# Performance work log

Measured on AMD Instinct MI355X. Metric: run time of the kernel, lower is better.

Reference implementation:

```python
import jax, jax.numpy as jnp
import numpy as np
import math

B, S, DIN, DOUT, H, L, R, E = 8, 512, 256, 256, 8, 4, 8, 65536
N = B * S  # graph nodes = all tokens
DEPTH = DOUT // H


def setup_inputs() -> dict:
    key = jax.random.key(0)
    ks = jax.random.split(key, 16)
    s_in = 1.0 / math.sqrt(DIN)
    s_out = 1.0 / math.sqrt(DOUT)
    return {
        "x": jax.random.normal(ks[0], (B, S, DIN), jnp.float32),
        # graph structure (constant ints)
        "edge_src": jax.random.randint(ks[1], (E,), 0, N),
        "edge_dst": jax.random.randint(ks[2], (E,), 0, N),
        "edge_type": jax.random.randint(ks[3], (E,), 0, R),
        # linear: input_size -> output_size
        "Wl": jax.random.normal(ks[4], (DOUT, DIN), jnp.float32) * s_in,
        "bl": jnp.zeros((DOUT,), jnp.float32),
        # relational GAT params per layer / relation
        "Wgat": jax.random.normal(ks[5], (L, R, DOUT, DOUT), jnp.float32) * s_out,
        "a_src": jax.random.normal(ks[6], (L, R, DOUT), jnp.float32) * s_out,
        "a_dst": jax.random.normal(ks[7], (L, R, DOUT), jnp.float32) * s_out,
        # linear1: output_size -> input_size
        "W1": jax.random.normal(ks[8], (DIN, DOUT), jnp.float32) * s_out,
        "b1": jnp.zeros((DIN,), jnp.float32),
        # Wq, Wk: input_size -> output_size
        "Wq": jax.random.normal(ks[9], (DOUT, DIN), jnp.float32) * s_in,
        "bq": jnp.zeros((DOUT,), jnp.float32),
        "Wk": jax.random.normal(ks[10], (DOUT, DIN), jnp.float32) * s_in,
        "bk": jnp.zeros((DOUT,), jnp.float32),
    }


def _segment_softmax(e, dst, n):
    m = jax.ops.segment_max(e, dst, num_segments=n)
    ex = jnp.exp(e - m[dst])
    denom = jax.ops.segment_sum(ex, dst, num_segments=n)
    return ex / (denom[dst] + 1e-16)


def _rgat(h, Wgat, a_src, a_dst, edge_src, edge_dst, edge_type):
    # h: [N, DOUT]
    for l in range(L):
        # per-relation transform of all nodes: [R, N, D]
        hr = jnp.einsum('nd,rde->rne', h, Wgat[l])
        msg = hr[edge_type, edge_src]  # [E, D] gather by (relation, src)
        logits = (jnp.sum(a_src[l][edge_type] * msg, axis=-1)
                  + jnp.sum(a_dst[l][edge_type] * h[edge_dst], axis=-1))
        alpha = _segment_softmax(jax.nn.leaky_relu(logits, 0.2), edge_dst, N)
        agg = jax.ops.segment_sum(alpha[:, None] * msg, edge_dst, num_segments=N)
        h = jax.nn.elu(agg)
    return h


def reference(x, edge_src, edge_dst, edge_type, Wl, bl, Wgat, a_src, a_dst,
              W1, b1, Wq, bq, Wk, bk):
    h = x @ Wl.T + bl                       # [B, S, DOUT]
    h = h.reshape(N, DOUT)
    h = _rgat(h, Wgat, a_src, a_dst, edge_src, edge_dst, edge_type)
    h = h.reshape(B, S, DOUT)
    h = h @ W1.T + b1                       # [B, S, DIN]
    q = (h @ Wq.T + bq).reshape(B, S, H, DEPTH).transpose(0, 2, 1, 3)
    k = (h @ Wk.T + bk).reshape(B, S, H, DEPTH).transpose(0, 2, 1, 3)
    attn = jnp.einsum('bhqd,bhkd->bhqk', q, k) / math.sqrt(DEPTH)
    return attn
```

## Files before the change

kernel.cpp:

```cpp
#include <hip/hip_runtime.h>
#include <math.h>

#define NN 4096
#define D 256
#define RR 8
#define LL 4
#define EE 65536
#define BB 8
#define SS 512
#define HH 8
#define RK 256
#define RN 2048

typedef short bf16x8 __attribute__((ext_vector_type(8)));
typedef float f32x4 __attribute__((ext_vector_type(4)));

__device__ __forceinline__ unsigned short f2bf(float f) {
  unsigned u = __float_as_uint(f);
  unsigned r = (u + 0x7fffu + ((u >> 16) & 1u)) >> 16;
  return (unsigned short)r;
}
__device__ __forceinline__ float bf2f(unsigned short s) {
  return __uint_as_float(((unsigned)s) << 16);
}

__device__ __forceinline__ void gload16(unsigned short* dst, const unsigned short* src) {
  __builtin_amdgcn_global_load_lds(
      (const __attribute__((address_space(1))) void*)src,
      (__attribute__((address_space(3))) void*)dst, 16, 0, 0);
}

template<int BM, int BN, bool F32OUT, bool SPLITOUT>
__device__ __forceinline__ void gemm_body(unsigned short* lds, int bx, int by,
    const unsigned short* __restrict__ Ah, const unsigned short* __restrict__ Al,
    const unsigned short* __restrict__ Bh, const unsigned short* __restrict__ Bl,
    const float* __restrict__ bias,
    float* __restrict__ C, unsigned short* __restrict__ Ch, unsigned short* __restrict__ Cl,
    int M, int N, int K)
{
  constexpr int MF = BM / 32;
  constexpr int NF = BN / 32;
  constexpr int ABUF = BM * 32;
  constexpr int BBUF = BN * 32;
  constexpr int BUFSZ = 2 * ABUF + 2 * BBUF;

  const int t = threadIdx.x;
  const int lane = t & 63;
  const int w = t >> 6;
  const int wm = w >> 1, wn = w & 1;
  const int rb = by * BM;
  const int cb = bx * BN;

  f32x4 acc[MF][NF];
#pragma unroll
  for (int m = 0; m < MF; ++m)
#pragma unroll
    for (int n = 0; n < NF; ++n)
      acc[m][n] = (f32x4){0.f, 0.f, 0.f, 0.f};

  const int srow = t >> 2;
  const int lslot = (t & 3) ^ ((srow >> 1) & 3);
  const unsigned short* gAh = Ah + (size_t)(rb + srow) * K + lslot * 8;
  const unsigned short* gAl = Al + (size_t)(rb + srow) * K + lslot * 8;
  const unsigned short* gBh = Bh + (size_t)(cb + srow) * K + lslot * 8;
  const unsigned short* gBl = Bl + (size_t)(cb + srow) * K + lslot * 8;

  auto stage = [&](int buf, int k0) {
    unsigned short* p = lds + buf * BUFSZ;
#pragma unroll
    for (int i = 0; i < BM / 64; ++i) {
      gload16(p + i * 2048 + t * 8,        gAh + (size_t)i * 64 * K + k0);
      gload16(p + ABUF + i * 2048 + t * 8, gAl + (size_t)i * 64 * K + k0);
    }
#pragma unroll
    for (int i = 0; i < BN / 64; ++i) {
      gload16(p + 2 * ABUF + i * 2048 + t * 8,        gBh + (size_t)i * 64 * K + k0);
      gload16(p + 2 * ABUF + BBUF + i * 2048 + t * 8, gBl + (size_t)i * 64 * K + k0);
    }
  };

  stage(0, 0);
  int cur = 0;
  for (int k0 = 0; k0 < K; k0 += 32) {
    __syncthreads();
    if (k0 + 32 < K) stage(cur ^ 1, k0 + 32);
    const unsigned short* p = lds + cur * BUFSZ;

    bf16x8 ah[MF], al[MF];
#pragma unroll
    for (int m = 0; m < MF; ++m) {
      int row = wm * (BM / 2) + m * 16 + (lane & 15);
      int off = row * 32 + (((lane >> 4) ^ ((row >> 1) & 3)) << 3);
      ah[m] = *(const bf16x8*)(p + off);
      al[m] = *(const bf16x8*)(p + ABUF + off);
    }
#pragma unroll
    for (int n = 0; n < NF; ++n) {
      int brow = wn * (BN / 2) + n * 16 + (lane & 15);
      int boff = brow * 32 + (((lane >> 4) ^ ((brow >> 1) & 3)) << 3);
      bf16x8 bh = *(const bf16x8*)(p + 2 * ABUF + boff);
      bf16x8 bl = *(const bf16x8*)(p + 2 * ABUF + BBUF + boff);
#pragma unroll
      for (int m = 0; m < MF; ++m) {
        acc[m][n] = __builtin_amdgcn_mfma_f32_16x16x32_bf16(ah[m], bh, acc[m][n], 0, 0, 0);
        acc[m][n] = __builtin_amdgcn_mfma_f32_16x16x32_bf16(al[m], bh, acc[m][n], 0, 0, 0);
        acc[m][n] = __builtin_amdgcn_mfma_f32_16x16x32_bf16(ah[m], bl, acc[m][n], 0, 0, 0);
      }
    }
    cur ^= 1;
  }

#pragma unroll
  for (int m = 0; m < MF; ++m) {
#pragma unroll
    for (int n = 0; n < NF; ++n) {
      int row0 = rb + wm * (BM / 2) + m * 16 + (lane >> 4) * 4;
      int col = cb + wn * (BN / 2) + n * 16 + (lane & 15);
      float bv = bias ? bias[col] : 0.f;
#pragma unroll
      for (int j = 0; j < 4; ++j) {
        float v = acc[m][n][j] + bv;
        size_t idx = (size_t)(row0 + j) * N + col;
        if (F32OUT) C[idx] = v;
        if (SPLITOUT) {
          unsigned short hb = f2bf(v);
          Ch[idx] = hb;
          Cl[idx] = f2bf(v - bf2f(hb));
        }
      }
    }
  }
}

template<int BM, int BN, bool F32OUT, bool SPLITOUT>
__global__ __launch_bounds__(256) void gemm_split(
    const unsigned short* __restrict__ Ah, const unsigned short* __restrict__ Al,
    const unsigned short* __restrict__ Bh, const unsigned short* __restrict__ Bl,
    const float* __restrict__ bias,
    float* __restrict__ C, unsigned short* __restrict__ Ch, unsigned short* __restrict__ Cl,
    int M, int N, int K)
{
  __shared__ unsigned short lds[2 * (2 * BM * 32 + 2 * BN * 32)];
  gemm_body<BM, BN, F32OUT, SPLITOUT>(lds, blockIdx.x, blockIdx.y,
      Ah, Al, Bh, Bl, bias, C, Ch, Cl, M, N, K);
}

__global__ __launch_bounds__(256) void fill_gemm1_k(
    const int* __restrict__ ed, int* __restrict__ cur, int* __restrict__ csr,
    const unsigned short* __restrict__ xh, const unsigned short* __restrict__ xl,
    const unsigned short* __restrict__ wlh, const unsigned short* __restrict__ wll,
    const float* __restrict__ bl,
    unsigned short* __restrict__ hh, unsigned short* __restrict__ hl)
{
  __shared__ unsigned short lds[2 * (2 * 64 * 32 + 2 * 64 * 32)];
  int b = blockIdx.x;
  if (b < 256) {
    int e = b * 256 + threadIdx.x;
    int p = atomicAdd(&cur[ed[e]], 1);
    csr[p] = e;
  } else {
    int b2 = b - 256;
    gemm_body<64, 64, false, true>(lds, b2 & 3, b2 >> 2,
        xh, xl, wlh, wll, bl, nullptr, hh, hl, NN, D, D);
  }
}

__global__ __launch_bounds__(256) void rgat_scores_k(
    const unsigned short* __restrict__ Ah, const unsigned short* __restrict__ Al,
    const unsigned short* __restrict__ Bh, const unsigned short* __restrict__ Bl,
    float* __restrict__ C,
    const float* __restrict__ wa_l, const float* __restrict__ adst_l,
    float* __restrict__ ssrc, float* __restrict__ sdst)
{
  __shared__ unsigned short lds[2 * (2 * 128 * 32 + 2 * 128 * 32)];
  const int b = blockIdx.x;
  const int t = threadIdx.x;
  if (b < 512) {
    gemm_body<128, 128, true, false>(lds, b & 15, b >> 4,
        Ah, Al, Bh, Bl, nullptr, C, nullptr, nullptr, NN, RN, RK);
  } else {
    float* sh = (float*)lds;
    int n = b - 512;
    size_t idx = (size_t)n * D + t;
    sh[t] = bf2f(Ah[idx]) + bf2f(Al[idx]);
    __syncthreads();
    int lane = t & 63, wv = t >> 6;
#pragma unroll
    for (int rr = 0; rr < 2; ++rr) {
      int r = wv * 2 + rr;
      const float* wr = wa_l + (size_t)r * D;
      const float* ar = adst_l + (size_t)r * D;
      float s1 = sh[lane] * wr[lane] + sh[lane+64] * wr[lane+64]
               + sh[lane+128] * wr[lane+128] + sh[lane+192] * wr[lane+192];
      float s2 = sh[lane] * ar[lane] + sh[lane+64] * ar[lane+64]
               + sh[lane+128] * ar[lane+128] + sh[lane+192] * ar[lane+192];
#pragma unroll
      for (int o = 32; o; o >>= 1) { s1 += __shfl_down(s1, o); s2 += __shfl_down(s2, o); }
      if (lane == 0) { ssrc[(size_t)r * NN + n] = s1; sdst[(size_t)r * NN + n] = s2; }
    }
  }
}

__global__ __launch_bounds__(1024) void scan_k(const int* __restrict__ cnt,
    int* __restrict__ off, int* __restrict__ cur) {
  __shared__ int part[1024];
  int t = threadIdx.x;
  int base = t * 4;
  int c0 = cnt[base], c1 = cnt[base+1], c2 = cnt[base+2], c3 = cnt[base+3];
  int s = c0 + c1 + c2 + c3;
  part[t] = s;
  __syncthreads();
  for (int o = 1; o < 1024; o <<= 1) {
    int v = 0;
    if (t >= o) v = part[t - o];
    __syncthreads();
    part[t] += v;
    __syncthreads();
  }
  int excl = part[t] - s;
  off[base] = excl; off[base+1] = excl + c0; off[base+2] = excl + c0 + c1;
  off[base+3] = excl + c0 + c1 + c2;
  cur[base] = excl; cur[base+1] = excl + c0; cur[base+2] = excl + c0 + c1;
  cur[base+3] = excl + c0 + c1 + c2;
  if (t == 1023) off[NN] = EE;
}

__global__ __launch_bounds__(256) void prep_k(
    const float* __restrict__ x, unsigned short* __restrict__ xh, unsigned short* __restrict__ xl,
    const float* __restrict__ Wl, unsigned short* __restrict__ wlh, unsigned short* __restrict__ wll,
    const float* __restrict__ Wq, const float* __restrict__ Wk, const float* __restrict__ W1,
    unsigned short* __restrict__ fqkh, unsigned short* __restrict__ fqkl,
    const float* __restrict__ b1, const float* __restrict__ bq, const float* __restrict__ bk,
    float* __restrict__ bqk,
    const float* __restrict__ Wgat, const float* __restrict__ asrc,
    unsigned short* __restrict__ th, unsigned short* __restrict__ tl,
    float* __restrict__ wa,
    const int* __restrict__ ed, int* __restrict__ cnt)
{
  __shared__ float s[32][33];
  int b = blockIdx.x, t = threadIdx.x;
  if (b < 1088) {
    const float* src; unsigned short* hi; unsigned short* lo; int i;
    if (b < 1024) { src = x;  hi = xh;  lo = xl;  i = b * 256 + t; }
    else          { src = Wl; hi = wlh; lo = wll; i = (b - 1024) * 256 + t; }
    float4 v = ((const float4*)src)[i];
    ushort4 h, l;
    h.x = f2bf(v.x); l.x = f2bf(v.x - bf2f(h.x));
    h.y = f2bf(v.y); l.y = f2bf(v.y - bf2f(h.y));
    h.z = f2bf(v.z); l.z = f2bf(v.z - bf2f(h.z));
    h.w = f2bf(v.w); l.w = f2bf(v.w - bf2f(h.w));
    ((ushort4*)hi)[i] = h;
    ((ushort4*)lo)[i] = l;
  } else if (b < 1600) {
    int b2 = b - 1088;
    int j = (b2 & 3) * 64 + (t & 63);
    int i = (b2 >> 2) * 4 + (t >> 6);
    const float* row = i < 256 ? Wq + (size_t)i * D : Wk + (size_t)(i - 256) * D;
    float sm = 0.f;
    for (int k = 0; k < D; ++k) sm += row[k] * W1[(size_t)k * D + j];
    size_t idx = (size_t)i * D + j;
    unsigned short hb = f2bf(sm);
    fqkh[idx] = hb;
    fqkl[idx] = f2bf(sm - bf2f(hb));
  } else if (b < 1728) {
    int b2 = b - 1600;
    int idx = b2 * 4 + (t >> 6);
    int lane = t & 63;
    const float* row = idx < 256 ? Wq + (size_t)idx * D : Wk + (size_t)(idx - 256) * D;
    float sm = 0.f;
    for (int i = lane; i < D; i += 64) sm += row[i] * b1[i];
#pragma unroll
    for (int o = 32; o; o >>= 1) sm += __shfl_down(sm, o);
    if (lane == 0) bqk[idx] = sm + (idx < 256 ? bq[idx] : bk[idx - 256]);
  } else if (b < 3776) {
    int b2 = b - 1728;
    int g = b2 >> 6, bi = (b2 >> 3) & 7, bj = b2 & 7;
    int r = t >> 3, c = (t & 7) * 4;
    float4 v = *(const float4*)(Wgat + ((size_t)g * D + bi * 32 + r) * D + bj * 32 + c);
    s[r][c + 0] = v.x; s[r][c + 1] = v.y; s[r][c + 2] = v.z; s[r][c + 3] = v.w;
    __syncthreads();
    size_t ob = ((size_t)g * D + bj * 32 + r) * D + bi * 32 + c;
    ushort4 h, l4;
    float o0 = s[c + 0][r], o1 = s[c + 1][r], o2 = s[c + 2][r], o3 = s[c + 3][r];
    h.x = f2bf(o0); l4.x = f2bf(o0 - bf2f(h.x));
    h.y = f2bf(o1); l4.y = f2bf(o1 - bf2f(h.y));
    h.z = f2bf(o2); l4.z = f2bf(o2 - bf2f(h.z));
    h.w = f2bf(o3); l4.w = f2bf(o3 - bf2f(h.w));
    *(ushort4*)(th + ob) = h;
    *(ushort4*)(tl + ob) = l4;
    if (t < 32) {
      const float* av = asrc + (size_t)g * D + bj * 32;
      float p2 = 0.f;
#pragma unroll
      for (int cc = 0; cc < 32; ++cc) p2 += s[t][cc] * av[cc];
      atomicAdd(&wa[(size_t)g * D + bi * 32 + t], p2);
    }
  } else {
    int e = (b - 3776) * 256 + t;
    atomicAdd(&cnt[ed[e]], 1);
  }
}

__global__ __launch_bounds__(256) void agg_fused_k(
    const int* __restrict__ csr, const int* __restrict__ off,
    const int* __restrict__ et, const int* __restrict__ es,
    const float* __restrict__ ssrc, const float* __restrict__ sdst,
    const float* __restrict__ hr2,
    unsigned short* __restrict__ hh, unsigned short* __restrict__ hl,
    const float* __restrict__ wa_next, const float* __restrict__ adst_next,
    float* __restrict__ ssrc_o, float* __restrict__ sdst_o)
{
  __shared__ float slog[1024];
  __shared__ int soff[1024];
  __shared__ float sdn[RR];
  __shared__ float red[8];
  __shared__ float wred[4][256];
  int n = blockIdx.x, tid = threadIdx.x;
  int o0 = off[n];
  int deg = off[n + 1] - o0;
  if (deg > 1024) deg = 1024;
  if (tid < RR) sdn[tid] = sdst[(size_t)tid * NN + n];
  __syncthreads();
  for (int i = tid; i < deg; i += 256) {
    int e = csr[o0 + i];
    int t = et[e], s = es[e];
    float v = ssrc[(size_t)t * NN + s] + sdn[t];
    slog[i] = v > 0.f ? v : 0.2f * v;
    soff[i] = s * (RR * D) + t * D;
  }
  __syncthreads();
  int lane = tid & 63, wv = tid >> 6;
  float lm = -INFINITY;
  for (int i = tid; i < deg; i += 256) lm = fmaxf(lm, slog[i]);
#pragma unroll
  for (int o = 32; o; o >>= 1) lm = fmaxf(lm, __shfl_xor(lm, o));
  if (lane == 0) red[wv] = lm;
  __syncthreads();
  float m = fmaxf(fmaxf(red[0], red[1]), fmaxf(red[2], red[3]));
  float ls = 0.f;
  for (int i = tid; i < deg; i += 256) {
    float a = expf(slog[i] - m);
    slog[i] = a;
    ls += a;
  }
#pragma unroll
  for (int o = 32; o; o >>= 1) ls += __shfl_xor(ls, o);
  if (lane == 0) red[4 + wv] = ls;
  __syncthreads();
  float dinv = 1.f / (red[4] + red[5] + red[6] + red[7] + 1e-16f);
  float4 a4 = make_float4(0.f, 0.f, 0.f, 0.f);
  for (int i = wv; i < deg; i += 4) {
    float al = slog[i];
    float4 rv = ((const float4*)(hr2 + (size_t)soff[i]))[lane];
    a4.x += al * rv.x; a4.y += al * rv.y; a4.z += al * rv.z; a4.w += al * rv.w;
  }
  ((float4*)wred[wv])[lane] = a4;
  __syncthreads();
  float acc = (wred[0][tid] + wred[1][tid]) + (wred[2][tid] + wred[3][tid]);
  acc *= dinv;
  float v = acc > 0.f ? acc : expm1f(acc);
  size_t idx = (size_t)n * D + tid;
  unsigned short hb = f2bf(v);
  hh[idx] = hb;
  hl[idx] = f2bf(v - bf2f(hb));

  if (wa_next) {
    __syncthreads();
    slog[tid] = v;
    __syncthreads();
#pragma unroll
    for (int rr2 = 0; rr2 < 2; ++rr2) {
      int r = wv * 2 + rr2;
      const float* wr = wa_next + (size_t)r * D;
      const float* ar = adst_next + (size_t)r * D;
      float s1 = slog[lane] * wr[lane] + slog[lane+64] * wr[lane+64]
               + slog[lane+128] * wr[lane+128] + slog[lane+192] * wr[lane+192];
      float s2 = slog[lane] * ar[lane] + slog[lane+64] * ar[lane+64]
               + slog[lane+128] * ar[lane+128] + slog[lane+192] * ar[lane+192];
#pragma unroll
      for (int o = 32; o; o >>= 1) { s1 += __shfl_down(s1, o); s2 += __shfl_down(s2, o); }
      if (lane == 0) { ssrc_o[(size_t)r * NN + n] = s1; sdst_o[(size_t)r * NN + n] = s2; }
    }
  }
}

__global__ __launch_bounds__(256) void attn_mfma_k(
    const unsigned short* __restrict__ qkh, const unsigned short* __restrict__ qkl,
    float* __restrict__ out)
{
  int bh = blockIdx.y; int b = bh >> 3, hd = bh & 7;
  int rb = (blockIdx.x >> 3) * 64, cb = (blockIdx.x & 7) * 64;
  int t = threadIdx.x, lane = t & 63, w = t >> 6;
  int wm = w >> 1, wn = w & 1;
  int colq = hd * 32 + (lane >> 4) * 8;
  int colk = 256 + colq;
  int arow = b * SS + rb + wm * 32 + (lane & 15);
  int brow = b * SS + cb + wn * 32 + (lane & 15);

  bf16x8 aH[2], aL[2], bH[2], bL[2];
#pragma unroll
  for (int m = 0; m < 2; ++m) {
    size_t o1 = (size_t)(arow + m * 16) * 512 + colq;
    aH[m] = *(const bf16x8*)(qkh + o1);
    aL[m] = *(const bf16x8*)(qkl + o1);
    size_t o2 = (size_t)(brow + m * 16) * 512 + colk;
    bH[m] = *(const bf16x8*)(qkh + o2);
    bL[m] = *(const bf16x8*)(qkl + o2);
  }
  f32x4 acc[2][2];
#pragma unroll
  for (int m = 0; m < 2; ++m)
#pragma unroll
    for (int n = 0; n < 2; ++n) {
      acc[m][n] = (f32x4){0.f, 0.f, 0.f, 0.f};
      acc[m][n] = __builtin_amdgcn_mfma_f32_16x16x32_bf16(aH[m], bH[n], acc[m][n], 0, 0, 0);
      acc[m][n] = __builtin_amdgcn_mfma_f32_16x16x32_bf16(aL[m], bH[n], acc[m][n], 0, 0, 0);
      acc[m][n] = __builtin_amdgcn_mfma_f32_16x16x32_bf16(aH[m], bL[n], acc[m][n], 0, 0, 0);
    }
  const float scale = 0.17677669529663687f;
  size_t ob = (size_t)bh * SS * SS;
#pragma unroll
  for (int m = 0; m < 2; ++m)
#pragma unroll
    for (int n = 0; n < 2; ++n) {
      int row0 = rb + wm * 32 + m * 16 + (lane >> 4) * 4;
      int col = cb + wn * 32 + n * 16 + (lane & 15);
#pragma unroll
      for (int j = 0; j < 4; ++j)
        out[ob + (size_t)(row0 + j) * SS + col] = acc[m][n][j] * scale;
    }
}

extern "C" void kernel_launch(void* const* d_in, const int* in_sizes, int n_in,
                              void* d_out, int out_size, void* d_ws, size_t ws_size,
                              hipStream_t stream) {
  const float* x    = (const float*)d_in[0];
  const int*   es   = (const int*)d_in[1];
  const int*   ed   = (const int*)d_in[2];
  const int*   et   = (const int*)d_in[3];
  const float* Wl   = (const float*)d_in[4];
  const float* bl   = (const float*)d_in[5];
  const float* Wgat = (const float*)d_in[6];
  const float* asr  = (const float*)d_in[7];
  const float* adt  = (const float*)d_in[8];
  const float* W1   = (const float*)d_in[9];
  const float* b1   = (const float*)d_in[10];
  const float* Wq   = (const float*)d_in[11];
  const float* bq   = (const float*)d_in[12];
  const float* Wk   = (const float*)d_in[13];
  const float* bk   = (const float*)d_in[14];
  float* out = (float*)d_out;

  char* w = (char*)d_ws;
  size_t o = 0;
  auto alloc = [&](size_t bytes) { void* p = w + o; o += (bytes + 255) & ~(size_t)255; return p; };
  unsigned short* hh    = (unsigned short*)alloc((size_t)NN * D * 2);
  unsigned short* hl    = (unsigned short*)alloc((size_t)NN * D * 2);
  unsigned short* Wgt_h = (unsigned short*)alloc((size_t)LL * RR * D * D * 2);
  unsigned short* Wgt_l = (unsigned short*)alloc((size_t)LL * RR * D * D * 2);
  unsigned short* wlh   = (unsigned short*)alloc((size_t)D * D * 2);
  unsigned short* wll   = (unsigned short*)alloc((size_t)D * D * 2);
  unsigned short* fqkh  = (unsigned short*)alloc((size_t)2 * D * D * 2);
  unsigned short* fqkl  = (unsigned short*)alloc((size_t)2 * D * D * 2);
  float* bqk   = (float*)alloc((size_t)2 * D * 4);
  int*   cnt   = (int*)alloc((size_t)NN * 4);
  float* wa    = (float*)alloc((size_t)LL * RR * D * 4);
  float* ssrcA = (float*)alloc((size_t)RR * NN * 4);
  float* sdstA = (float*)alloc((size_t)RR * NN * 4);
  float* ssrcB = (float*)alloc((size_t)RR * NN * 4);
  float* sdstB = (float*)alloc((size_t)RR * NN * 4);
  int*   off   = (int*)alloc((size_t)(NN + 1) * 4);
  int*   cur   = (int*)alloc((size_t)NN * 4);
  int*   csr   = (int*)alloc((size_t)EE * 4);
  char* big = (char*)alloc((size_t)NN * RR * D * 4);
  float*          hr2 = (float*)big;
  unsigned short* xh  = (unsigned short*)big;
  unsigned short* xl  = (unsigned short*)(big + (size_t)NN * D * 2);
  unsigned short* qkh = (unsigned short*)big;
  unsigned short* qkl = (unsigned short*)(big + (size_t)NN * 512 * 2);

  hipMemsetAsync(cnt, 0, (size_t)NN * 4 + (size_t)LL * RR * D * 4, stream);

  prep_k<<<4032, 256, 0, stream>>>(x, xh, xl, Wl, wlh, wll, Wq, Wk, W1,
                                   fqkh, fqkl, b1, bq, bk, bqk,
                                   Wgat, asr, Wgt_h, Wgt_l, wa, ed, cnt);
  scan_k<<<1, 1024, 0, stream>>>(cnt, off, cur);
  fill_gemm1_k<<<512, 256, 0, stream>>>(ed, cur, csr, xh, xl, wlh, wll, bl, hh, hl);

  for (int l = 0; l < LL; ++l) {
    int grid = (l == 0) ? 512 + NN : 512;
    rgat_scores_k<<<grid, 256, 0, stream>>>(
        hh, hl, Wgt_h + (size_t)l * RR * D * D, Wgt_l + (size_t)l * RR * D * D,
        hr2, wa, adt, ssrcA, sdstA);
    const float* wan = (l < LL - 1) ? wa + (size_t)(l + 1) * RR * D : nullptr;
    const float* adn = (l < LL - 1) ? adt + (size_t)(l + 1) * RR * D : nullptr;
    const float* sin_ = (l & 1) ? ssrcB : ssrcA;
    const float* din_ = (l & 1) ? sdstB : sdstA;
    float* sou_ = (l & 1) ? ssrcA : ssrcB;
    float* dou_ = (l & 1) ? sdstA : sdstB;
    agg_fused_k<<<NN, 256, 0, stream>>>(csr, off, et, es, sin_, din_, hr2,
                                        hh, hl, wan, adn, sou_, dou_);
  }

  gemm_split<64, 64, false, true><<<dim3(8, 64), 256, 0, stream>>>(
      hh, hl, fqkh, fqkl, bqk, nullptr, qkh, qkl, NN, 512, D);

  attn_mfma_k<<<dim3(64, BB * HH), 256, 0, stream>>>(qkh, qkl, out);
}
```

Measured before the change: 221.1 us.

## Swizzle GEMM block order, warp-shuffle scan, unroll edge aggregation loop

Three independent changes. The relational-score GEMM now remaps block indices so consecutive blocks walk a different tile order, aiming at better L2 reuse. The prefix scan switches from a 1024-step LDS Hillis-Steele loop with many barriers to wavefront shuffles plus a 16-entry serial pass. The aggregation loop handles two edges per iteration with separate accumulators to raise memory-level parallelism on the gathers, which changes floating-point summation order slightly.

```diff
diff --git a/kernel.cpp b/kernel.cpp
--- a/kernel.cpp
+++ b/kernel.cpp
@@ -176,7 +176,8 @@
   const int b = blockIdx.x;
   const int t = threadIdx.x;
   if (b < 512) {
-    gemm_body<128, 128, true, false>(lds, b & 15, b >> 4,
+    int tb = (b & 7) * 64 + (b >> 3);
+    gemm_body<128, 128, true, false>(lds, tb & 15, tb >> 4,
         Ah, Al, Bh, Bl, nullptr, C, nullptr, nullptr, NN, RN, RK);
   } else {
     float* sh = (float*)lds;
@@ -203,21 +204,27 @@
 
 __global__ __launch_bounds__(1024) void scan_k(const int* __restrict__ cnt,
     int* __restrict__ off, int* __restrict__ cur) {
-  __shared__ int part[1024];
+  __shared__ int wsum[16];
   int t = threadIdx.x;
+  int lane = t & 63, wv = t >> 6;
   int base = t * 4;
   int c0 = cnt[base], c1 = cnt[base+1], c2 = cnt[base+2], c3 = cnt[base+3];
   int s = c0 + c1 + c2 + c3;
-  part[t] = s;
-  __syncthreads();
-  for (int o = 1; o < 1024; o <<= 1) {
-    int v = 0;
-    if (t >= o) v = part[t - o];
-    __syncthreads();
-    part[t] += v;
-    __syncthreads();
-  }
-  int excl = part[t] - s;
+  int run = s;
+#pragma unroll
+  for (int o = 1; o < 64; o <<= 1) {
+    int v = __shfl_up(run, o);
+    if (lane >= o) run += v;
+  }
+  if (lane == 63) wsum[wv] = run;
+  __syncthreads();
+  if (t == 0) {
+    int r = 0;
+#pragma unroll
+    for (int i = 0; i < 16; ++i) { int x = wsum[i]; wsum[i] = r; r += x; }
+  }
+  __syncthreads();
+  int excl = wsum[wv] + run - s;
   off[base] = excl; off[base+1] = excl + c0; off[base+2] = excl + c0 + c1;
   off[base+3] = excl + c0 + c1 + c2;
   cur[base] = excl; cur[base+1] = excl + c0; cur[base+2] = excl + c0 + c1;
@@ -349,11 +356,21 @@
   __syncthreads();
   float dinv = 1.f / (red[4] + red[5] + red[6] + red[7] + 1e-16f);
   float4 a4 = make_float4(0.f, 0.f, 0.f, 0.f);
-  for (int i = wv; i < deg; i += 4) {
-    float al = slog[i];
-    float4 rv = ((const float4*)(hr2 + (size_t)soff[i]))[lane];
-    a4.x += al * rv.x; a4.y += al * rv.y; a4.z += al * rv.z; a4.w += al * rv.w;
-  }
+  float4 b4 = make_float4(0.f, 0.f, 0.f, 0.f);
+  int i = wv;
+  for (; i + 4 < deg; i += 8) {
+    float al0 = slog[i], al1 = slog[i + 4];
+    float4 r0 = ((const float4*)(hr2 + (size_t)soff[i]))[lane];
+    float4 r1 = ((const float4*)(hr2 + (size_t)soff[i + 4]))[lane];
+    a4.x += al0 * r0.x; a4.y += al0 * r0.y; a4.z += al0 * r0.z; a4.w += al0 * r0.w;
+    b4.x += al1 * r1.x; b4.y += al1 * r1.y; b4.z += al1 * r1.z; b4.w += al1 * r1.w;
+  }
+  if (i < deg) {
+    float al0 = slog[i];
+    float4 r0 = ((const float4*)(hr2 + (size_t)soff[i]))[lane];
+    a4.x += al0 * r0.x; a4.y += al0 * r0.y; a4.z += al0 * r0.z; a4.w += al0 * r0.w;
+  }
+  a4.x += b4.x; a4.y += b4.y; a4.z += b4.z; a4.w += b4.w;
   ((float4*)wred[wv])[lane] = a4;
   __syncthreads();
   float acc = (wred[0][tid] + wred[1][tid]) + (wred[2][tid] + wred[3][tid]);
```

New measurement: 218.3 us (median of 3 runs). No clear change (-1.3%).
